# Kernel tuning notes

Measured on AMD Instinct MI355X. Metric: run time of the kernel, lower is better.

## Reference

```python
import jax, jax.numpy as jnp
import numpy as np

EPS = 1e-05


def layer_norm(x, scale):
    # Faithful to source bug: returns scale * x_norm + scale (shift param unused)
    mean = jnp.mean(x, axis=-1, keepdims=True)
    var = jnp.var(x, axis=-1, keepdims=True)  # unbiased=False
    x_norm = (x - mean) / jnp.sqrt(var + EPS)
    return scale * x_norm + scale


def mhsa(x, wq, wk, wv, wo, bo, n_heads):
    b, t, d = x.shape
    hd = d // n_heads
    # torch Linear: y = x @ W.T (no qkv bias)
    q = (x @ wq.T).reshape(b, t, n_heads, hd).transpose(0, 2, 1, 3)  # bhtd
    k = (x @ wk.T).reshape(b, t, n_heads, hd).transpose(0, 2, 1, 3)
    v = (x @ wv.T).reshape(b, t, n_heads, hd).transpose(0, 2, 1, 3)
    scores = jnp.einsum('bhqd,bhkd->bhqk', q, k)
    causal = jnp.triu(jnp.ones((t, t), dtype=bool), k=1)
    scores = jnp.where(causal, -jnp.inf, scores)
    attn = jax.nn.softmax(scores / np.sqrt(hd).astype(np.float32), axis=-1)
    ctx = jnp.einsum('bhqk,bhkd->bhqd', attn, v)
    ctx = ctx.transpose(0, 2, 1, 3).reshape(b, t, d)
    return ctx @ wo.T + bo


def setup_inputs() -> dict:
    key = jax.random.key(0)
    ks = jax.random.split(key, 6)
    B, T, D = 2, 2048, 1024
    return {
        'x': jax.random.normal(ks[0], (B, T, D), dtype=jnp.float32),
        'wq': jax.random.normal(ks[1], (D, D), dtype=jnp.float32) * 0.02,
        'wk': jax.random.normal(ks[2], (D, D), dtype=jnp.float32) * 0.02,
        'wv': jax.random.normal(ks[3], (D, D), dtype=jnp.float32) * 0.02,
        'wo': jax.random.normal(ks[4], (D, D), dtype=jnp.float32) * 0.02,
        'bo': jnp.zeros((D,), dtype=jnp.float32),
        'ln1_scale': jnp.ones((D,), dtype=jnp.float32),
        'ln2_scale': jnp.ones((D,), dtype=jnp.float32),
    }


def reference(x, wq, wk, wv, wo, bo, ln1_scale, ln2_scale):
    n_heads = 16
    # Block 1: norm1 -> attn -> (+residual); dropout is identity in eval mode
    h = x + mhsa(layer_norm(x, ln1_scale), wq, wk, wv, wo, bo, n_heads)
    # Block 2: source calls self.attn (same weights) again, not self.ff
    out = h + mhsa(layer_norm(h, ln2_scale), wq, wk, wv, wo, bo, n_heads)
    return out
```

## Files before the change

### kernel.cpp

```cpp
#include <hip/hip_runtime.h>
#include <hip/hip_bf16.h>
#include <math.h>

#define Dm 1024
#define Tm 2048
#define Bm 2
#define Hm 16
#define HDm 64
#define Rm (Bm*Tm)
#define QS 3072

typedef __attribute__((ext_vector_type(8))) short sh8;
typedef __attribute__((ext_vector_type(4))) float f32x4;

#define AS1(p) ((const __attribute__((address_space(1))) void*)(p))
#define AS3(p) ((__attribute__((address_space(3))) void*)(p))

__device__ __forceinline__ short f2bs(float f) {
    union { float f; unsigned u; } v; v.f = f;
    unsigned r = v.u + 0x7FFFu + ((v.u >> 16) & 1u);
    return (short)(r >> 16);
}

__global__ __launch_bounds__(256) void convert_w(const float* __restrict__ wq,
                                                 const float* __restrict__ wk,
                                                 const float* __restrict__ wv,
                                                 const float* __restrict__ wo,
                                                 short* __restrict__ wqkv,
                                                 short* __restrict__ wob) {
    int idx = (blockIdx.x * 256 + threadIdx.x) * 4;
    const int M1 = 1 << 20;
    const float* src; short* dst; int off;
    if (idx < M1)           { src = wq; dst = wqkv;          off = idx; }
    else if (idx < 2*M1)    { src = wk; dst = wqkv + M1;     off = idx - M1; }
    else if (idx < 3*M1)    { src = wv; dst = wqkv + 2*M1;   off = idx - 2*M1; }
    else                    { src = wo; dst = wob;           off = idx - 3*M1; }
    float4 v = *(const float4*)(src + off);
    short4 o;
    o.x = f2bs(v.x); o.y = f2bs(v.y); o.z = f2bs(v.z); o.w = f2bs(v.w);
    *(short4*)(dst + off) = o;
}

__global__ __launch_bounds__(256) void ln_kernel(const float* __restrict__ x,
                                                 const float* __restrict__ scale,
                                                 short* __restrict__ out) {
    int row = blockIdx.x;
    int t = threadIdx.x;
    const float4* xr = (const float4*)(x + (size_t)row * Dm);
    float4 v = xr[t];
    float s  = v.x + v.y + v.z + v.w;
    float ss = v.x*v.x + v.y*v.y + v.z*v.z + v.w*v.w;
    #pragma unroll
    for (int off = 32; off; off >>= 1) {
        s  += __shfl_xor(s, off);
        ss += __shfl_xor(ss, off);
    }
    __shared__ float red[8];
    int wave = t >> 6, lane = t & 63;
    if (lane == 0) { red[wave*2] = s; red[wave*2+1] = ss; }
    __syncthreads();
    s  = red[0] + red[2] + red[4] + red[6];
    ss = red[1] + red[3] + red[5] + red[7];
    float mean = s * (1.0f / Dm);
    float var  = ss * (1.0f / Dm) - mean * mean;
    float rstd = 1.0f / sqrtf(var + 1e-5f);
    float4 sc = ((const float4*)scale)[t];
    short4 o;
    o.x = f2bs(sc.x * ((v.x - mean) * rstd) + sc.x);
    o.y = f2bs(sc.y * ((v.y - mean) * rstd) + sc.y);
    o.z = f2bs(sc.z * ((v.z - mean) * rstd) + sc.z);
    o.w = f2bs(sc.w * ((v.w - mean) * rstd) + sc.w);
    ((short4*)(out + (size_t)row * Dm))[t] = o;
}

template<int BN, bool BF16OUT>
__global__ __launch_bounds__(256) void gemm_mfma(const short* __restrict__ A,
                                                 const short* __restrict__ B,
                                                 const float* __restrict__ bias,
                                                 const float* __restrict__ res,
                                                 void* __restrict__ Cv,
                                                 int M, int N, int K) {
    __shared__ short As[128*32];
    __shared__ short Bs[BN*32];
    const int NJ = BN / 32;
    int t = threadIdx.x;
    int lane = t & 63, w = t >> 6;
    int l = lane & 15, quad = lane >> 4;
    int wm = (w & 1) * 64, wn = (w >> 1) * (BN/2);
    int m0 = blockIdx.y * 128, n0 = blockIdx.x * BN;

    f32x4 acc[4][NJ];
    #pragma unroll
    for (int i = 0; i < 4; i++)
        #pragma unroll
        for (int j = 0; j < NJ; j++)
            acc[i][j] = (f32x4){0.f,0.f,0.f,0.f};

    for (int k0 = 0; k0 < K; k0 += 32) {
        __syncthreads();
        #pragma unroll
        for (int p = 0; p < 2; p++) {
            int off = p*4096 + t*16;
            int row = off >> 6;
            int c = ((off >> 4) & 3) ^ (row & 3);
            const short* ga = A + (size_t)(m0 + row) * K + k0 + c*8;
            __builtin_amdgcn_global_load_lds(AS1(ga), AS3((char*)As + off), 16, 0, 0);
        }
        #pragma unroll
        for (int p = 0; p < BN/64; p++) {
            int off = p*4096 + t*16;
            int row = off >> 6;
            int c = ((off >> 4) & 3) ^ (row & 3);
            const short* gb = B + (size_t)(n0 + row) * K + k0 + c*8;
            __builtin_amdgcn_global_load_lds(AS1(gb), AS3((char*)Bs + off), 16, 0, 0);
        }
        __syncthreads();
        sh8 af[4], bf[NJ];
        #pragma unroll
        for (int i = 0; i < 4; i++) {
            int m = wm + i*16 + l;
            af[i] = *(const sh8*)((const char*)As + m*64 + ((quad ^ (m & 3)) * 16));
        }
        #pragma unroll
        for (int j = 0; j < NJ; j++) {
            int n = wn + j*16 + l;
            bf[j] = *(const sh8*)((const char*)Bs + n*64 + ((quad ^ (n & 3)) * 16));
        }
        #pragma unroll
        for (int i = 0; i < 4; i++)
            #pragma unroll
            for (int j = 0; j < NJ; j++)
                acc[i][j] = __builtin_amdgcn_mfma_f32_16x16x32_bf16(af[i], bf[j], acc[i][j], 0, 0, 0);
    }
    #pragma unroll
    for (int i = 0; i < 4; i++) {
        #pragma unroll
        for (int j = 0; j < NJ; j++) {
            #pragma unroll
            for (int r = 0; r < 4; r++) {
                int m = m0 + wm + i*16 + quad*4 + r;
                int n = n0 + wn + j*16 + l;
                float vv = acc[i][j][r];
                if (BF16OUT) {
                    ((short*)Cv)[(size_t)m * N + n] = f2bs(vv);
                } else {
                    vv += bias[n] + res[(size_t)m * N + n];
                    ((float*)Cv)[(size_t)m * N + n] = vv;
                }
            }
        }
    }
}

#define KP 72

__global__ __launch_bounds__(256) void attn_mfma(const short* __restrict__ qkv,
                                                 short* __restrict__ ctx) {
    __shared__ short Kl[64*64];
    __shared__ short Vt[64*KP];
    __shared__ short Pl[4][16*KP];
    int t = threadIdx.x;
    int lane = t & 63, w = t >> 6;
    int l = lane & 15, quad = lane >> 4;
    int pair = blockIdx.x;
    int bh = blockIdx.y;
    int b = bh >> 4, h = bh & 15;
    size_t rbase = (size_t)b * Tm;
    const short* qp0 = qkv + rbase * QS + h*HDm;
    const short* kp0 = qp0 + Dm;
    const short* vp0 = qp0 + 2*Dm;

    for (int ph = 0; ph < 2; ph++) {
        int qt = ph ? (31 - pair) : pair;
        int qtbase = qt * 64;

        sh8 qf0, qf1;
        {
            const short* qp = qp0 + (size_t)(qtbase + w*16 + l) * QS + quad*8;
            qf0 = *(const sh8*)qp;
            qf1 = *(const sh8*)(qp + 32);
        }
        f32x4 O[4] = {{0,0,0,0},{0,0,0,0},{0,0,0,0},{0,0,0,0}};
        float psum = 0.f;

        for (int kc = 0; kc <= qt; kc++) {
            int kbase = kc * 64;
            __syncthreads();
            #pragma unroll
            for (int p = 0; p < 2; p++) {
                int off = p*4096 + t*16;
                int key = off >> 7;
                int c = ((off >> 4) & 7) ^ (key & 7);
                const short* g = kp0 + (size_t)(kbase + key) * QS + c*8;
                __builtin_amdgcn_global_load_lds(AS1(g), AS3((char*)Kl + off), 16, 0, 0);
            }
            {
                int d = t & 63;
                const short* vp = vp0 + (size_t)(kbase + w*16) * QS + d;
                sh8 t0, t1;
                #pragma unroll
                for (int i = 0; i < 8; i++) t0[i] = vp[(size_t)i * QS];
                #pragma unroll
                for (int i = 0; i < 8; i++) t1[i] = vp[(size_t)(i+8) * QS];
                *(sh8*)&Vt[d*KP + w*16]     = t0;
                *(sh8*)&Vt[d*KP + w*16 + 8] = t1;
            }
            __syncthreads();

            f32x4 S[4];
            #pragma unroll
            for (int kt = 0; kt < 4; kt++) {
                const f32x4 z = {0.f,0.f,0.f,0.f};
                int key = kt*16 + l;
                const char* kb = (const char*)Kl + key*128;
                int sw = key & 7;
                sh8 k0 = *(const sh8*)(kb + ((quad ^ sw) * 16));
                sh8 k1 = *(const sh8*)(kb + (((4 + quad) ^ sw) * 16));
                f32x4 s = __builtin_amdgcn_mfma_f32_16x16x32_bf16(k0, qf0, z, 0, 0, 0);
                s = __builtin_amdgcn_mfma_f32_16x16x32_bf16(k1, qf1, s, 0, 0, 0);
                S[kt] = s;
            }
            bool needmask = (kbase + 63 > qtbase + w*16);
            int qrow = qtbase + w*16 + l;
            #pragma unroll
            for (int kt = 0; kt < 4; kt++) {
                float p[4];
                if (needmask) {
                    #pragma unroll
                    for (int r = 0; r < 4; r++) {
                        int key = kbase + kt*16 + quad*4 + r;
                        p[r] = (key > qrow) ? 0.f : __expf(S[kt][r] * 0.125f);
                        psum += p[r];
                    }
                } else {
                    #pragma unroll
                    for (int r = 0; r < 4; r++) {
                        p[r] = __expf(S[kt][r] * 0.125f);
                        psum += p[r];
                    }
                }
                __hip_bfloat162 pa = __float22bfloat162_rn({p[0], p[1]});
                __hip_bfloat162 pb = __float22bfloat162_rn({p[2], p[3]});
                union { __hip_bfloat162 h[2]; short4 s4; } u;
                u.h[0] = pa; u.h[1] = pb;
                *(short4*)&Pl[w][l*KP + kt*16 + quad*4] = u.s4;
            }
            sh8 p0 = *(const sh8*)&Pl[w][l*KP + quad*8];
            sh8 p1 = *(const sh8*)&Pl[w][l*KP + 32 + quad*8];
            #pragma unroll
            for (int dt = 0; dt < 4; dt++) {
                sh8 v0 = *(const sh8*)&Vt[(dt*16+l)*KP + quad*8];
                sh8 v1 = *(const sh8*)&Vt[(dt*16+l)*KP + 32 + quad*8];
                O[dt] = __builtin_amdgcn_mfma_f32_16x16x32_bf16(p0, v0, O[dt], 0, 0, 0);
                O[dt] = __builtin_amdgcn_mfma_f32_16x16x32_bf16(p1, v1, O[dt], 0, 0, 0);
            }
        }
        psum += __shfl_xor(psum, 16);
        psum += __shfl_xor(psum, 32);
        #pragma unroll
        for (int r = 0; r < 4; r++) {
            int src = (lane & 48) | (((lane >> 4) << 2) + r);
            float inv = 1.0f / __shfl(psum, src);
            int row = qtbase + w*16 + quad*4 + r;
            #pragma unroll
            for (int dt = 0; dt < 4; dt++)
                ctx[(rbase + row) * Dm + h*HDm + dt*16 + l] = f2bs(O[dt][r] * inv);
        }
    }
}

extern "C" void kernel_launch(void* const* d_in, const int* in_sizes, int n_in,
                              void* d_out, int out_size, void* d_ws, size_t ws_size,
                              hipStream_t stream) {
    const float* x   = (const float*)d_in[0];
    const float* wq  = (const float*)d_in[1];
    const float* wk  = (const float*)d_in[2];
    const float* wv  = (const float*)d_in[3];
    const float* wo  = (const float*)d_in[4];
    const float* bo  = (const float*)d_in[5];
    const float* ln1 = (const float*)d_in[6];
    const float* ln2 = (const float*)d_in[7];
    float* out = (float*)d_out;

    short* lnb  = (short*)d_ws;
    short* ctxb = lnb + (size_t)Rm*Dm;
    short* qkv  = ctxb + (size_t)Rm*Dm;
    short* wqkv = qkv + (size_t)Rm*QS;
    short* wob  = wqkv + (size_t)3*Dm*Dm;

    dim3 qgrid(QS/128, Rm/128);
    dim3 pgrid(Dm/64,  Rm/128);
    dim3 agrid(16, Bm*Hm);

    convert_w<<<4096, 256, 0, stream>>>(wq, wk, wv, wo, wqkv, wob);

    ln_kernel<<<Rm, 256, 0, stream>>>(x, ln1, lnb);
    gemm_mfma<128, true><<<qgrid, 256, 0, stream>>>(lnb, wqkv, nullptr, nullptr, qkv, Rm, QS, Dm);
    attn_mfma<<<agrid, 256, 0, stream>>>(qkv, ctxb);
    gemm_mfma<64, false><<<pgrid, 256, 0, stream>>>(ctxb, wob, bo, x, out, Rm, Dm, Dm);

    ln_kernel<<<Rm, 256, 0, stream>>>(out, ln2, lnb);
    gemm_mfma<128, true><<<qgrid, 256, 0, stream>>>(lnb, wqkv, nullptr, nullptr, qkv, Rm, QS, Dm);
    attn_mfma<<<agrid, 256, 0, stream>>>(qkv, ctxb);
    gemm_mfma<64, false><<<pgrid, 256, 0, stream>>>(ctxb, wob, bo, out, out, Rm, Dm, Dm);
}
```

Before: 328.7 us.

## Pre-transpose V, fold softmax scale into Q projection, compute row sums via MFMA

Adds a transpose_v kernel that writes V as head-major [d][t], so the attention kernel can stream V tiles into LDS with async global_load_lds instead of doing strided scalar gathers. The QKV GEMM epilogue now multiplies Q by 0.125*log2(e), which lets the softmax use a bare exp2. Row sums are accumulated with an extra MFMA against a ones vector instead of per-lane adds plus shuffles. The grid changes from 16 paired blocks (each handling a short and a long query tile) to 32 blocks of one query tile each, processed longest first, which trades the explicit load pairing for scheduler balancing and adds an extra kernel launch plus a V round-trip through memory.

```diff
diff --git a/kernel.cpp b/kernel.cpp
--- a/kernel.cpp
+++ b/kernel.cpp
@@ -20,6 +20,14 @@
     union { float f; unsigned u; } v; v.f = f;
     unsigned r = v.u + 0x7FFFu + ((v.u >> 16) & 1u);
     return (short)(r >> 16);
+}
+
+__device__ __forceinline__ float fexp2(float x) {
+#if __has_builtin(__builtin_amdgcn_exp2f)
+    return __builtin_amdgcn_exp2f(x);
+#else
+    return exp2f(x);
+#endif
 }
 
 __global__ __launch_bounds__(256) void convert_w(const float* __restrict__ wq,
@@ -79,7 +87,7 @@
                                                  const float* __restrict__ bias,
                                                  const float* __restrict__ res,
                                                  void* __restrict__ Cv,
-                                                 int M, int N, int K) {
+                                                 int M, int N, int K, float qsc) {
     __shared__ short As[128*32];
     __shared__ short Bs[BN*32];
     const int NJ = BN / 32;
@@ -132,6 +140,7 @@
             for (int j = 0; j < NJ; j++)
                 acc[i][j] = __builtin_amdgcn_mfma_f32_16x16x32_bf16(af[i], bf[j], acc[i][j], 0, 0, 0);
     }
+    float sc = (BF16OUT && n0 < Dm) ? qsc : 1.0f;
     #pragma unroll
     for (int i = 0; i < 4; i++) {
         #pragma unroll
@@ -142,7 +151,7 @@
                 int n = n0 + wn + j*16 + l;
                 float vv = acc[i][j][r];
                 if (BF16OUT) {
-                    ((short*)Cv)[(size_t)m * N + n] = f2bs(vv);
+                    ((short*)Cv)[(size_t)m * N + n] = f2bs(vv * sc);
                 } else {
                     vv += bias[n] + res[(size_t)m * N + n];
                     ((float*)Cv)[(size_t)m * N + n] = vv;
@@ -152,120 +161,136 @@
     }
 }
 
-#define KP 72
+__global__ __launch_bounds__(256) void transpose_v(const short* __restrict__ qkv,
+                                                   short* __restrict__ vT) {
+    __shared__ short Tl[64][72];
+    int bh = blockIdx.y;
+    int b = bh >> 4, h = bh & 15;
+    int t0 = blockIdx.x * 64;
+    int tid = threadIdx.x;
+    int tt = tid >> 2, dg = tid & 3;
+    const short* src = qkv + ((size_t)(b*Tm + t0 + tt)) * QS + 2*Dm + h*HDm + dg*16;
+    *(sh8*)&Tl[tt][dg*16]     = *(const sh8*)src;
+    *(sh8*)&Tl[tt][dg*16 + 8] = *(const sh8*)(src + 8);
+    __syncthreads();
+    #pragma unroll
+    for (int ph = 0; ph < 2; ph++) {
+        int d = (tid >> 3) + ph*32;
+        int c = tid & 7;
+        sh8 o;
+        #pragma unroll
+        for (int j = 0; j < 8; j++) o[j] = Tl[c*8 + j][d];
+        *(sh8*)(vT + ((size_t)bh*HDm + d)*Tm + t0 + c*8) = o;
+    }
+}
 
 __global__ __launch_bounds__(256) void attn_mfma(const short* __restrict__ qkv,
+                                                 const short* __restrict__ vT,
                                                  short* __restrict__ ctx) {
     __shared__ short Kl[64*64];
-    __shared__ short Vt[64*KP];
-    __shared__ short Pl[4][16*KP];
+    __shared__ short Vl[64*64];
+    __shared__ short Pl[4][16*72];
     int t = threadIdx.x;
     int lane = t & 63, w = t >> 6;
     int l = lane & 15, quad = lane >> 4;
-    int pair = blockIdx.x;
+    int qt = 31 - blockIdx.x;
     int bh = blockIdx.y;
     int b = bh >> 4, h = bh & 15;
+    int qtbase = qt * 64;
     size_t rbase = (size_t)b * Tm;
     const short* qp0 = qkv + rbase * QS + h*HDm;
     const short* kp0 = qp0 + Dm;
-    const short* vp0 = qp0 + 2*Dm;
-
-    for (int ph = 0; ph < 2; ph++) {
-        int qt = ph ? (31 - pair) : pair;
-        int qtbase = qt * 64;
-
-        sh8 qf0, qf1;
-        {
-            const short* qp = qp0 + (size_t)(qtbase + w*16 + l) * QS + quad*8;
-            qf0 = *(const sh8*)qp;
-            qf1 = *(const sh8*)(qp + 32);
-        }
-        f32x4 O[4] = {{0,0,0,0},{0,0,0,0},{0,0,0,0},{0,0,0,0}};
-        float psum = 0.f;
-
-        for (int kc = 0; kc <= qt; kc++) {
-            int kbase = kc * 64;
-            __syncthreads();
-            #pragma unroll
-            for (int p = 0; p < 2; p++) {
-                int off = p*4096 + t*16;
-                int key = off >> 7;
-                int c = ((off >> 4) & 7) ^ (key & 7);
-                const short* g = kp0 + (size_t)(kbase + key) * QS + c*8;
-                __builtin_amdgcn_global_load_lds(AS1(g), AS3((char*)Kl + off), 16, 0, 0);
+    const short* vt0 = vT + (size_t)bh * HDm * Tm;
+
+    sh8 qf0, qf1;
+    {
+        const short* qp = qp0 + (size_t)(qtbase + w*16 + l) * QS + quad*8;
+        qf0 = *(const sh8*)qp;
+        qf1 = *(const sh8*)(qp + 32);
+    }
+    const short oneb = 0x3F80;
+    sh8 ones = {oneb, oneb, oneb, oneb, oneb, oneb, oneb, oneb};
+
+    f32x4 O[4] = {{0,0,0,0},{0,0,0,0},{0,0,0,0},{0,0,0,0}};
+    f32x4 L = {0,0,0,0};
+    int qrow = qtbase + w*16 + l;
+
+    for (int kc = 0; kc <= qt; kc++) {
+        int kbase = kc * 64;
+        __syncthreads();
+        #pragma unroll
+        for (int p = 0; p < 2; p++) {
+            int off = p*4096 + t*16;
+            int row = off >> 7;
+            int c = ((off >> 4) & 7) ^ (row & 7);
+            const short* g = kp0 + (size_t)(kbase + row) * QS + c*8;
+            __builtin_amdgcn_global_load_lds(AS1(g), AS3((char*)Kl + off), 16, 0, 0);
+        }
+        #pragma unroll
+        for (int p = 0; p < 2; p++) {
+            int off = p*4096 + t*16;
+            int row = off >> 7;
+            int c = ((off >> 4) & 7) ^ (row & 7);
+            const short* g = vt0 + (size_t)row * Tm + kbase + c*8;
+            __builtin_amdgcn_global_load_lds(AS1(g), AS3((char*)Vl + off), 16, 0, 0);
+        }
+        __syncthreads();
+
+        f32x4 S[4];
+        #pragma unroll
+        for (int kt = 0; kt < 4; kt++) {
+            const f32x4 z = {0.f,0.f,0.f,0.f};
+            int key = kt*16 + l;
+            const char* kb = (const char*)Kl + key*128;
+            int sw = key & 7;
+            sh8 k0 = *(const sh8*)(kb + ((quad ^ sw) * 16));
+            sh8 k1 = *(const sh8*)(kb + (((4 + quad) ^ sw) * 16));
+            f32x4 s = __builtin_amdgcn_mfma_f32_16x16x32_bf16(k0, qf0, z, 0, 0, 0);
+            s = __builtin_amdgcn_mfma_f32_16x16x32_bf16(k1, qf1, s, 0, 0, 0);
+            S[kt] = s;
+        }
+        bool needmask = (kbase + 63 > qtbase + w*16);
+        #pragma unroll
+        for (int kt = 0; kt < 4; kt++) {
+            float p[4];
+            if (needmask) {
+                #pragma unroll
+                for (int r = 0; r < 4; r++) {
+                    int key = kbase + kt*16 + quad*4 + r;
+                    p[r] = (key > qrow) ? 0.f : fexp2(S[kt][r]);
+                }
+            } else {
+                #pragma unroll
+                for (int r = 0; r < 4; r++) p[r] = fexp2(S[kt][r]);
             }
-            {
-                int d = t & 63;
-                const short* vp = vp0 + (size_t)(kbase + w*16) * QS + d;
-                sh8 t0, t1;
-                #pragma unroll
-                for (int i = 0; i < 8; i++) t0[i] = vp[(size_t)i * QS];
-                #pragma unroll
-                for (int i = 0; i < 8; i++) t1[i] = vp[(size_t)(i+8) * QS];
-                *(sh8*)&Vt[d*KP + w*16]     = t0;
-                *(sh8*)&Vt[d*KP + w*16 + 8] = t1;
-            }
-            __syncthreads();
-
-            f32x4 S[4];
-            #pragma unroll
-            for (int kt = 0; kt < 4; kt++) {
-                const f32x4 z = {0.f,0.f,0.f,0.f};
-                int key = kt*16 + l;
-                const char* kb = (const char*)Kl + key*128;
-                int sw = key & 7;
-                sh8 k0 = *(const sh8*)(kb + ((quad ^ sw) * 16));
-                sh8 k1 = *(const sh8*)(kb + (((4 + quad) ^ sw) * 16));
-                f32x4 s = __builtin_amdgcn_mfma_f32_16x16x32_bf16(k0, qf0, z, 0, 0, 0);
-                s = __builtin_amdgcn_mfma_f32_16x16x32_bf16(k1, qf1, s, 0, 0, 0);
-                S[kt] = s;
-            }
-            bool needmask = (kbase + 63 > qtbase + w*16);
-            int qrow = qtbase + w*16 + l;
-            #pragma unroll
-            for (int kt = 0; kt < 4; kt++) {
-                float p[4];
-                if (needmask) {
-                    #pragma unroll
-                    for (int r = 0; r < 4; r++) {
-                        int key = kbase + kt*16 + quad*4 + r;
-                        p[r] = (key > qrow) ? 0.f : __expf(S[kt][r] * 0.125f);
-                        psum += p[r];
-                    }
-                } else {
-                    #pragma unroll
-                    for (int r = 0; r < 4; r++) {
-                        p[r] = __expf(S[kt][r] * 0.125f);
-                        psum += p[r];
-                    }
-                }
-                __hip_bfloat162 pa = __float22bfloat162_rn({p[0], p[1]});
-                __hip_bfloat162 pb = __float22bfloat162_rn({p[2], p[3]});
-                union { __hip_bfloat162 h[2]; short4 s4; } u;
-                u.h[0] = pa; u.h[1] = pb;
-                *(short4*)&Pl[w][l*KP + kt*16 + quad*4] = u.s4;
-            }
-            sh8 p0 = *(const sh8*)&Pl[w][l*KP + quad*8];
-            sh8 p1 = *(const sh8*)&Pl[w][l*KP + 32 + quad*8];
-            #pragma unroll
-            for (int dt = 0; dt < 4; dt++) {
-                sh8 v0 = *(const sh8*)&Vt[(dt*16+l)*KP + quad*8];
-                sh8 v1 = *(const sh8*)&Vt[(dt*16+l)*KP + 32 + quad*8];
-                O[dt] = __builtin_amdgcn_mfma_f32_16x16x32_bf16(p0, v0, O[dt], 0, 0, 0);
-                O[dt] = __builtin_amdgcn_mfma_f32_16x16x32_bf16(p1, v1, O[dt], 0, 0, 0);
-            }
-        }
-        psum += __shfl_xor(psum, 16);
-        psum += __shfl_xor(psum, 32);
-        #pragma unroll
-        for (int r = 0; r < 4; r++) {
-            int src = (lane & 48) | (((lane >> 4) << 2) + r);
-            float inv = 1.0f / __shfl(psum, src);
-            int row = qtbase + w*16 + quad*4 + r;
-            #pragma unroll
-            for (int dt = 0; dt < 4; dt++)
-                ctx[(rbase + row) * Dm + h*HDm + dt*16 + l] = f2bs(O[dt][r] * inv);
-        }
+            __hip_bfloat162 pa = __float22bfloat162_rn({p[0], p[1]});
+            __hip_bfloat162 pb = __float22bfloat162_rn({p[2], p[3]});
+            union { __hip_bfloat162 h[2]; short4 s4; } u;
+            u.h[0] = pa; u.h[1] = pb;
+            *(short4*)&Pl[w][l*72 + kt*16 + quad*4] = u.s4;
+        }
+        sh8 p0 = *(const sh8*)&Pl[w][l*72 + quad*8];
+        sh8 p1 = *(const sh8*)&Pl[w][l*72 + 32 + quad*8];
+        #pragma unroll
+        for (int dt = 0; dt < 4; dt++) {
+            int row = dt*16 + l;
+            const char* vb = (const char*)Vl + row*128;
+            int sw = row & 7;
+            sh8 v0 = *(const sh8*)(vb + ((quad ^ sw) * 16));
+            sh8 v1 = *(const sh8*)(vb + (((4 + quad) ^ sw) * 16));
+            O[dt] = __builtin_amdgcn_mfma_f32_16x16x32_bf16(p0, v0, O[dt], 0, 0, 0);
+            O[dt] = __builtin_amdgcn_mfma_f32_16x16x32_bf16(p1, v1, O[dt], 0, 0, 0);
+        }
+        L = __builtin_amdgcn_mfma_f32_16x16x32_bf16(p0, ones, L, 0, 0, 0);
+        L = __builtin_amdgcn_mfma_f32_16x16x32_bf16(p1, ones, L, 0, 0, 0);
+    }
+    #pragma unroll
+    for (int r = 0; r < 4; r++) {
+        float inv = 1.0f / L[r];
+        int row = qtbase + w*16 + quad*4 + r;
+        #pragma unroll
+        for (int dt = 0; dt < 4; dt++)
+            ctx[(rbase + row) * Dm + h*HDm + dt*16 + l] = f2bs(O[dt][r] * inv);
     }
 }
 
@@ -283,24 +308,30 @@
     float* out = (float*)d_out;
 
     short* lnb  = (short*)d_ws;
+    short* vT   = lnb;
     short* ctxb = lnb + (size_t)Rm*Dm;
     short* qkv  = ctxb + (size_t)Rm*Dm;
     short* wqkv = qkv + (size_t)Rm*QS;
     short* wob  = wqkv + (size_t)3*Dm*Dm;
 
+    const float qsc = 0.125f * 1.44269504f;
+
     dim3 qgrid(QS/128, Rm/128);
     dim3 pgrid(Dm/64,  Rm/128);
-    dim3 agrid(16, Bm*Hm);
+    dim3 agrid(32, Bm*Hm);
+    dim3 tgrid(Tm/64, Bm*Hm);
 
     convert_w<<<4096, 256, 0, stream>>>(wq, wk, wv, wo, wqkv, wob);
 
     ln_kernel<<<Rm, 256, 0, stream>>>(x, ln1, lnb);
-    gemm_mfma<128, true><<<qgrid, 256, 0, stream>>>(lnb, wqkv, nullptr, nullptr, qkv, Rm, QS, Dm);
-    attn_mfma<<<agrid, 256, 0, stream>>>(qkv, ctxb);
-    gemm_mfma<64, false><<<pgrid, 256, 0, stream>>>(ctxb, wob, bo, x, out, Rm, Dm, Dm);
+    gemm_mfma<128, true><<<qgrid, 256, 0, stream>>>(lnb, wqkv, nullptr, nullptr, qkv, Rm, QS, Dm, qsc);
+    transpose_v<<<tgrid, 256, 0, stream>>>(qkv, vT);
+    attn_mfma<<<agrid, 256, 0, stream>>>(qkv, vT, ctxb);
+    gemm_mfma<64, false><<<pgrid, 256, 0, stream>>>(ctxb, wob, bo, x, out, Rm, Dm, Dm, 1.0f);
 
     ln_kernel<<<Rm, 256, 0, stream>>>(out, ln2, lnb);
-    gemm_mfma<128, true><<<qgrid, 256, 0, stream>>>(lnb, wqkv, nullptr, nullptr, qkv, Rm, QS, Dm);
-    attn_mfma<<<agrid, 256, 0, stream>>>(qkv, ctxb);
-    gemm_mfma<64, false><<<pgrid, 256, 0, stream>>>(ctxb, wob, bo, out, out, Rm, Dm, Dm);
-}
+    gemm_mfma<128, true><<<qgrid, 256, 0, stream>>>(lnb, wqkv, nullptr, nullptr, qkv, Rm, QS, Dm, qsc);
+    transpose_v<<<tgrid, 256, 0, stream>>>(qkv, vT);
+    attn_mfma<<<agrid, 256, 0, stream>>>(qkv, vT, ctxb);
+    gemm_mfma<64, false><<<pgrid, 256, 0, stream>>>(ctxb, wob, bo, out, out, Rm, Dm, Dm, 1.0f);
+}
```

After: 350.6 us. 1.07x slower.
